# Optimization experiments

Measured on AMD Instinct MI355X. Metric: run time of the kernel, lower is better.

The kernel has to match this reference:

```python
import jax, jax.numpy as jnp
import numpy as np

B, S, D = 8, 4096, 64
LN_EPS = 1e-3  # keras LayerNormalization default epsilon


def setup_inputs() -> dict:
    key = jax.random.key(0)
    k1, k2 = jax.random.split(key)
    x = jax.random.normal(k1, (B, S, D), dtype=jnp.float32)
    # (D,D,D) concept tensor, scaled small like glorot-ish init
    concept_map = jax.random.normal(k2, (D, D, D), dtype=jnp.float32) * 0.02
    gamma = jnp.ones((D,), dtype=jnp.float32)
    beta = jnp.zeros((D,), dtype=jnp.float32)
    return {"x": x, "concept_map": concept_map, "gamma": gamma, "beta": beta}


def reference(x, concept_map, gamma, beta):
    b, s, d = x.shape
    # Causal Toeplitz decay matrix: T[i, j] = 1/(i-j)^2 for j < i, else 0.
    idx = jnp.arange(s)
    diff = idx[:, None] - idx[None, :]  # (S, S)
    T = jnp.where(diff > 0, 1.0 / (jnp.maximum(diff, 1).astype(x.dtype) ** 2), 0.0)
    # Weighted causal prefix sum: S_pre[b, i, c] = sum_{j<i} x[b, j, c] / (i-j)^2
    s_pre = jnp.einsum('ij,bjc->bic', T, x)
    # Bilinear form with concept tensor: out[b,i,k] = sum_{a,c} x[b,i,a] * s_pre[b,i,c] * W[k,a,c]
    outer = (x[:, :, :, None] * s_pre[:, :, None, :]).reshape(b, s, d * d)  # (B,S,D*D)
    out = outer @ concept_map.reshape(d, d * d).T  # (B,S,D)
    # Residual + LayerNorm (axis=-1, keras defaults). Dropout is identity at inference.
    r = out + x
    mu = jnp.mean(r, axis=-1, keepdims=True)
    var = jnp.mean((r - mu) ** 2, axis=-1, keepdims=True)
    y = (r - mu) / jnp.sqrt(var + LN_EPS) * gamma + beta
    return y
```

## Files before the change

### kernel.cpp

```cpp
#include <hip/hip_runtime.h>

#define S_DIM 4096
#define B_DIM 8
#define LN_EPS 1e-3f

typedef _Float16 half8 __attribute__((ext_vector_type(8)));
typedef _Float16 half2v __attribute__((ext_vector_type(2)));
typedef float f32x4 __attribute__((ext_vector_type(4)));

__global__ __launch_bounds__(256) void prep_stage1(const float* __restrict__ x,
                                                   const float* __restrict__ W,
                                                   _Float16* __restrict__ wt2,
                                                   _Float16* __restrict__ s_out) {
    if (blockIdx.x < 1024) {
        int idx = blockIdx.x * 256 + threadIdx.x;
        int a = idx >> 12;
        int j = (idx >> 9) & 7;
        int l2 = (idx >> 3) & 63;
        int e = idx & 7;
        int k = (j >> 1) * 16 + (l2 & 15);
        int c = (j & 1) * 32 + (l2 >> 4) * 8 + e;
        wt2[idx] = (_Float16)W[((k << 6) + a) * 64 + c];
        return;
    }
    const int lin = blockIdx.x - 1024;
    const int it = lin & 63;
    const int by = lin >> 6;
    const int i0 = it * 64;
    const int tid = threadIdx.x;
    const int w = tid >> 6, l = tid & 63, lg = l >> 4, lr = l & 15;

    __shared__ _Float16 Bs[64 * 72];

    f32x4 acc[4] = {};
    const float iRowF = (float)(i0 + w * 16 + lr);
    const int ldC = tid & 63;
    const int ldJ = (tid >> 6) * 16;

    const int jt0 = (it >= 2) ? (it - 2) : 0;
    for (int jt = jt0; jt <= it; ++jt) {
        const int j0 = jt * 64;
        __syncthreads();
        {
            const float* xp = x + ((size_t)by * S_DIM + j0 + ldJ) * 64 + ldC;
            half8 v0, v1;
            #pragma unroll
            for (int q = 0; q < 8; ++q) {
                v0[q] = (_Float16)xp[q * 64];
                v1[q] = (_Float16)xp[(8 + q) * 64];
            }
            *(half8*)&Bs[ldC * 72 + ldJ] = v0;
            *(half8*)&Bs[ldC * 72 + ldJ + 8] = v1;
        }
        __syncthreads();
        #pragma unroll
        for (int kk = 0; kk < 2; ++kk) {
            half8 af;
            #pragma unroll
            for (int bq = 0; bq < 8; ++bq) {
                int j = j0 + kk * 32 + lg * 8 + bq;
                float df = iRowF - (float)j;
                float tv = (df > 0.f) ? __builtin_amdgcn_rcpf(df * df) : 0.f;
                af[bq] = (_Float16)tv;
            }
            #pragma unroll
            for (int nt = 0; nt < 4; ++nt) {
                half8 bf = *(const half8*)&Bs[(nt * 16 + lr) * 72 + kk * 32 + lg * 8];
                acc[nt] = __builtin_amdgcn_mfma_f32_16x16x32_f16(af, bf, acc[nt], 0, 0, 0);
            }
        }
    }

    #pragma unroll
    for (int nt = 0; nt < 4; ++nt)
        #pragma unroll
        for (int r = 0; r < 4; ++r)
            s_out[((size_t)by * S_DIM + i0 + w * 16 + lg * 4 + r) * 64 + nt * 16 + lr]
                = (_Float16)acc[nt][r];
}

__global__ __launch_bounds__(256, 2) void stage2(const float* __restrict__ x,
                                                 const _Float16* __restrict__ s,
                                                 const _Float16* __restrict__ wt2,
                                                 const float* __restrict__ gamma,
                                                 const float* __restrict__ beta,
                                                 float* __restrict__ out) {
    const int r0 = blockIdx.x * 64;
    const int tid = threadIdx.x;
    const int w = tid >> 6, l = tid & 63, lg = l >> 4, lr = l & 15;

    __shared__ __align__(16) half2v Pf[6144];

    const char* mylane = (const char*)wt2 + ((size_t)w << 17) + l * 16;

    half8 sf[4][2];
    #pragma unroll
    for (int rt = 0; rt < 4; ++rt) {
        size_t row = (size_t)(r0 + rt * 16 + lr) * 64;
        sf[rt][0] = *(const half8*)&s[row + lg * 8];
        sf[rt][1] = *(const half8*)&s[row + 32 + lg * 8];
    }
    half8 xav[4][2];
    #pragma unroll
    for (int rt = 0; rt < 4; ++rt) {
        const float* xp = x + (size_t)(r0 + rt * 16 + lr) * 64 + w * 16;
        half8 h0, h1;
        #pragma unroll
        for (int j = 0; j < 8; ++j) {
            h0[j] = (_Float16)xp[j];
            h1[j] = (_Float16)xp[8 + j];
        }
        xav[rt][0] = h0;
        xav[rt][1] = h1;
    }

    half8 bA[4][2], bB[4][2];

#define PREF(BUF, t_)                                                          \
    {                                                                          \
        _Pragma("unroll")                                                      \
        for (int f_ = 0; f_ < 8; ++f_)                                         \
            (&BUF[0][0])[f_] =                                                 \
                *(const half8*)(mylane + (size_t)(t_) * 8192 + f_ * 1024);     \
    }
#define CLUSTER(BUF, t_)                                                       \
    {                                                                          \
        _Pragma("unroll")                                                      \
        for (int rt_ = 0; rt_ < 4; ++rt_) {                                    \
            _Float16 xa = xav[rt_][(t_) >> 3][(t_) & 7];                       \
            half8 af0 = sf[rt_][0] * xa;                                       \
            half8 af1 = sf[rt_][1] * xa;                                       \
            _Pragma("unroll")                                                  \
            for (int nt_ = 0; nt_ < 4; ++nt_) {                                \
                acc[rt_][nt_] = __builtin_amdgcn_mfma_f32_16x16x32_f16(        \
                    af0, BUF[nt_][0], acc[rt_][nt_], 0, 0, 0);                 \
                acc[rt_][nt_] = __builtin_amdgcn_mfma_f32_16x16x32_f16(        \
                    af1, BUF[nt_][1], acc[rt_][nt_], 0, 0, 0);                 \
            }                                                                  \
        }                                                                      \
    }

    f32x4 acc[4][4] = {};
    PREF(bA, 0);
    #pragma unroll
    for (int tt = 0; tt < 8; ++tt) {
        const int t0 = tt * 2;
        PREF(bB, t0 + 1);
        CLUSTER(bA, t0);
        if (t0 + 2 < 16) PREF(bA, t0 + 2);
        CLUSTER(bB, t0 + 1);
    }
#undef PREF
#undef CLUSTER

    if (w != 0) {
        const int ph = w - 1;
        #pragma unroll
        for (int rt = 0; rt < 4; ++rt)
            #pragma unroll
            for (int nt = 0; nt < 4; ++nt) {
                int base = (((ph * 4 + rt) * 4 + nt) * 2) * 64 + l;
                half2v p01 = { (_Float16)acc[rt][nt][0], (_Float16)acc[rt][nt][1] };
                half2v p23 = { (_Float16)acc[rt][nt][2], (_Float16)acc[rt][nt][3] };
                Pf[base] = p01;
                Pf[base + 64] = p23;
            }
    }
    __syncthreads();

    if (w == 0) {
        float gba[4], bta[4];
        #pragma unroll
        for (int nt = 0; nt < 4; ++nt) {
            gba[nt] = gamma[nt * 16 + lr];
            bta[nt] = beta[nt * 16 + lr];
        }
        #pragma unroll
        for (int rt = 0; rt < 4; ++rt) {
            float rv[4][4], sum[4], ssq[4];
            #pragma unroll
            for (int nt = 0; nt < 4; ++nt) {
                float v0 = acc[rt][nt][0], v1 = acc[rt][nt][1];
                float v2 = acc[rt][nt][2], v3 = acc[rt][nt][3];
                #pragma unroll
                for (int ph = 0; ph < 3; ++ph) {
                    int base = (((ph * 4 + rt) * 4 + nt) * 2) * 64 + l;
                    half2v q01 = Pf[base];
                    half2v q23 = Pf[base + 64];
                    v0 += (float)q01[0]; v1 += (float)q01[1];
                    v2 += (float)q23[0]; v3 += (float)q23[1];
                }
                acc[rt][nt][0] = v0; acc[rt][nt][1] = v1;
                acc[rt][nt][2] = v2; acc[rt][nt][3] = v3;
            }
            #pragma unroll
            for (int reg = 0; reg < 4; ++reg) {
                const int row_l = rt * 16 + lg * 4 + reg;
                const float* xr = x + (size_t)(r0 + row_l) * 64;
                float s_ = 0.f, q_ = 0.f;
                #pragma unroll
                for (int nt = 0; nt < 4; ++nt) {
                    float v = acc[rt][nt][reg] + xr[nt * 16 + lr];
                    rv[nt][reg] = v;
                    s_ += v;
                    q_ += v * v;
                }
                sum[reg] = s_;
                ssq[reg] = q_;
            }
            #pragma unroll
            for (int m = 1; m < 16; m <<= 1) {
                #pragma unroll
                for (int reg = 0; reg < 4; ++reg) {
                    sum[reg] += __shfl_xor(sum[reg], m, 64);
                    ssq[reg] += __shfl_xor(ssq[reg], m, 64);
                }
            }
            #pragma unroll
            for (int reg = 0; reg < 4; ++reg) {
                float mean = sum[reg] * (1.f / 64.f);
                float var = ssq[reg] * (1.f / 64.f) - mean * mean;
                float rstd = __frsqrt_rn(var + LN_EPS);
                const int gr = r0 + rt * 16 + lg * 4 + reg;
                #pragma unroll
                for (int nt = 0; nt < 4; ++nt) {
                    float y = (rv[nt][reg] - mean) * rstd * gba[nt] + bta[nt];
                    out[(size_t)gr * 64 + nt * 16 + lr] = y;
                }
            }
        }
    }
}

extern "C" void kernel_launch(void* const* d_in, const int* in_sizes, int n_in,
                              void* d_out, int out_size, void* d_ws, size_t ws_size,
                              hipStream_t stream) {
    const float* x     = (const float*)d_in[0];
    const float* W     = (const float*)d_in[1];
    const float* gamma = (const float*)d_in[2];
    const float* beta  = (const float*)d_in[3];
    float* outp        = (float*)d_out;

    char* ws = (char*)d_ws;
    _Float16* s_f16 = (_Float16*)ws;
    _Float16* wt2   = (_Float16*)(ws + (size_t)B_DIM * S_DIM * 64 * 2);

    prep_stage1<<<1536, 256, 0, stream>>>(x, W, wt2, s_f16);
    stage2<<<(B_DIM * S_DIM) / 64, 256, 0, stream>>>(x, s_f16, wt2, gamma, beta, outp);
}
```

Before: 34.61 us.

## Widen stage2 to 128 rows x 8 waves with LDS staging and tree reduction

The bilinear stage2 kernel now processes 128 rows per block with 8 waves, each handling 8 of the 64 'a' slices instead of 16. The s and x tiles are staged through swizzled LDS rather than held in registers. Each weight fragment loaded from global memory is reused across twice as many rows, which halves weight traffic per row. Per-wave partial sums are combined by a multi-step LDS tree reduction, and the LayerNorm epilogue is spread across all waves with vectorized loads and stores. In exchange the block uses about 68KB of LDS, has more barriers, and doubles the accumulator registers per thread, which may limit occupancy.

```diff
diff --git a/kernel.cpp b/kernel.cpp
--- a/kernel.cpp
+++ b/kernel.cpp
@@ -5,7 +5,7 @@
 #define LN_EPS 1e-3f
 
 typedef _Float16 half8 __attribute__((ext_vector_type(8)));
-typedef _Float16 half2v __attribute__((ext_vector_type(2)));
+typedef _Float16 half4v __attribute__((ext_vector_type(4)));
 typedef float f32x4 __attribute__((ext_vector_type(4)));
 
 __global__ __launch_bounds__(256) void prep_stage1(const float* __restrict__ x,
@@ -79,43 +79,25 @@
                 = (_Float16)acc[nt][r];
 }
 
-__global__ __launch_bounds__(256, 2) void stage2(const float* __restrict__ x,
+__global__ __launch_bounds__(512, 2) void stage2(const float* __restrict__ x,
                                                  const _Float16* __restrict__ s,
                                                  const _Float16* __restrict__ wt2,
                                                  const float* __restrict__ gamma,
                                                  const float* __restrict__ beta,
                                                  float* __restrict__ out) {
-    const int r0 = blockIdx.x * 64;
+    const int r0 = blockIdx.x * 128;
     const int tid = threadIdx.x;
     const int w = tid >> 6, l = tid & 63, lg = l >> 4, lr = l & 15;
 
-    __shared__ __align__(16) half2v Pf[6144];
-
-    const char* mylane = (const char*)wt2 + ((size_t)w << 17) + l * 16;
-
-    half8 sf[4][2];
-    #pragma unroll
-    for (int rt = 0; rt < 4; ++rt) {
-        size_t row = (size_t)(r0 + rt * 16 + lr) * 64;
-        sf[rt][0] = *(const half8*)&s[row + lg * 8];
-        sf[rt][1] = *(const half8*)&s[row + 32 + lg * 8];
-    }
-    half8 xav[4][2];
-    #pragma unroll
-    for (int rt = 0; rt < 4; ++rt) {
-        const float* xp = x + (size_t)(r0 + rt * 16 + lr) * 64 + w * 16;
-        half8 h0, h1;
-        #pragma unroll
-        for (int j = 0; j < 8; ++j) {
-            h0[j] = (_Float16)xp[j];
-            h1[j] = (_Float16)xp[8 + j];
-        }
-        xav[rt][0] = h0;
-        xav[rt][1] = h1;
-    }
+    __shared__ __align__(16) char smem[69632];
+    _Float16* sT = (_Float16*)smem;
+    _Float16* xT = (_Float16*)(smem + 16384);
+
+#define TB(q_) ((_Float16*)(smem + (q_) * 17408))
+
+    const char* mylane = (const char*)wt2 + ((size_t)w << 16) + l * 16;
 
     half8 bA[4][2], bB[4][2];
-
 #define PREF(BUF, t_)                                                          \
     {                                                                          \
         _Pragma("unroll")                                                      \
@@ -123,13 +105,44 @@
             (&BUF[0][0])[f_] =                                                 \
                 *(const half8*)(mylane + (size_t)(t_) * 8192 + f_ * 1024);     \
     }
+
+    PREF(bA, 0);
+
+    {
+        #pragma unroll
+        for (int h = 0; h < 2; ++h) {
+            int slot = h * 512 + tid;
+            int row = slot >> 3, c0 = (slot & 7) * 8;
+            half8 sv = *(const half8*)&s[(size_t)(r0 + row) * 64 + c0];
+            *(half8*)&sT[row * 64 + ((((c0 >> 3) ^ (row & 7))) << 3)] = sv;
+            const float* xp = x + (size_t)(r0 + row) * 64 + c0;
+            float4 v0 = *(const float4*)xp;
+            float4 v1 = *(const float4*)(xp + 4);
+            half8 hv;
+            hv[0] = (_Float16)v0.x; hv[1] = (_Float16)v0.y;
+            hv[2] = (_Float16)v0.z; hv[3] = (_Float16)v0.w;
+            hv[4] = (_Float16)v1.x; hv[5] = (_Float16)v1.y;
+            hv[6] = (_Float16)v1.z; hv[7] = (_Float16)v1.w;
+            *(half8*)&xT[row * 72 + c0] = hv;
+        }
+    }
+    __syncthreads();
+
+    const int sw0 = ((lg ^ (lr & 7)) << 3);
+    const int sw1 = (((4 + lg) ^ (lr & 7)) << 3);
+
+    f32x4 acc[8][4] = {};
+
 #define CLUSTER(BUF, t_)                                                       \
     {                                                                          \
         _Pragma("unroll")                                                      \
-        for (int rt_ = 0; rt_ < 4; ++rt_) {                                    \
-            _Float16 xa = xav[rt_][(t_) >> 3][(t_) & 7];                       \
-            half8 af0 = sf[rt_][0] * xa;                                       \
-            half8 af1 = sf[rt_][1] * xa;                                       \
+        for (int rt_ = 0; rt_ < 8; ++rt_) {                                    \
+            const int row_ = rt_ * 16 + lr;                                    \
+            _Float16 xa = xT[row_ * 72 + w * 8 + (t_)];                        \
+            half8 s0 = *(const half8*)&sT[row_ * 64 + sw0];                    \
+            half8 s1 = *(const half8*)&sT[row_ * 64 + sw1];                    \
+            half8 af0 = s0 * xa;                                               \
+            half8 af1 = s1 * xa;                                               \
             _Pragma("unroll")                                                  \
             for (int nt_ = 0; nt_ < 4; ++nt_) {                                \
                 acc[rt_][nt_] = __builtin_amdgcn_mfma_f32_16x16x32_f16(        \
@@ -140,96 +153,95 @@
         }                                                                      \
     }
 
-    f32x4 acc[4][4] = {};
-    PREF(bA, 0);
     #pragma unroll
-    for (int tt = 0; tt < 8; ++tt) {
+    for (int tt = 0; tt < 4; ++tt) {
         const int t0 = tt * 2;
         PREF(bB, t0 + 1);
         CLUSTER(bA, t0);
-        if (t0 + 2 < 16) PREF(bA, t0 + 2);
+        if (t0 + 2 < 8) PREF(bA, t0 + 2);
         CLUSTER(bB, t0 + 1);
     }
 #undef PREF
 #undef CLUSTER
 
-    if (w != 0) {
-        const int ph = w - 1;
-        #pragma unroll
-        for (int rt = 0; rt < 4; ++rt)
-            #pragma unroll
-            for (int nt = 0; nt < 4; ++nt) {
-                int base = (((ph * 4 + rt) * 4 + nt) * 2) * 64 + l;
-                half2v p01 = { (_Float16)acc[rt][nt][0], (_Float16)acc[rt][nt][1] };
-                half2v p23 = { (_Float16)acc[rt][nt][2], (_Float16)acc[rt][nt][3] };
-                Pf[base] = p01;
-                Pf[base + 64] = p23;
-            }
-    }
-    __syncthreads();
-
-    if (w == 0) {
-        float gba[4], bta[4];
-        #pragma unroll
-        for (int nt = 0; nt < 4; ++nt) {
-            gba[nt] = gamma[nt * 16 + lr];
-            bta[nt] = beta[nt * 16 + lr];
-        }
-        #pragma unroll
-        for (int rt = 0; rt < 4; ++rt) {
-            float rv[4][4], sum[4], ssq[4];
-            #pragma unroll
-            for (int nt = 0; nt < 4; ++nt) {
-                float v0 = acc[rt][nt][0], v1 = acc[rt][nt][1];
-                float v2 = acc[rt][nt][2], v3 = acc[rt][nt][3];
-                #pragma unroll
-                for (int ph = 0; ph < 3; ++ph) {
-                    int base = (((ph * 4 + rt) * 4 + nt) * 2) * 64 + l;
-                    half2v q01 = Pf[base];
-                    half2v q23 = Pf[base + 64];
-                    v0 += (float)q01[0]; v1 += (float)q01[1];
-                    v2 += (float)q23[0]; v3 += (float)q23[1];
-                }
-                acc[rt][nt][0] = v0; acc[rt][nt][1] = v1;
-                acc[rt][nt][2] = v2; acc[rt][nt][3] = v3;
-            }
-            #pragma unroll
-            for (int reg = 0; reg < 4; ++reg) {
-                const int row_l = rt * 16 + lg * 4 + reg;
-                const float* xr = x + (size_t)(r0 + row_l) * 64;
-                float s_ = 0.f, q_ = 0.f;
-                #pragma unroll
-                for (int nt = 0; nt < 4; ++nt) {
-                    float v = acc[rt][nt][reg] + xr[nt * 16 + lr];
-                    rv[nt][reg] = v;
-                    s_ += v;
-                    q_ += v * v;
-                }
-                sum[reg] = s_;
-                ssq[reg] = q_;
-            }
-            #pragma unroll
-            for (int m = 1; m < 16; m <<= 1) {
-                #pragma unroll
-                for (int reg = 0; reg < 4; ++reg) {
-                    sum[reg] += __shfl_xor(sum[reg], m, 64);
-                    ssq[reg] += __shfl_xor(ssq[reg], m, 64);
-                }
-            }
-            #pragma unroll
-            for (int reg = 0; reg < 4; ++reg) {
-                float mean = sum[reg] * (1.f / 64.f);
-                float var = ssq[reg] * (1.f / 64.f) - mean * mean;
-                float rstd = __frsqrt_rn(var + LN_EPS);
-                const int gr = r0 + rt * 16 + lg * 4 + reg;
-                #pragma unroll
-                for (int nt = 0; nt < 4; ++nt) {
-                    float y = (rv[nt][reg] - mean) * rstd * gba[nt] + bta[nt];
-                    out[(size_t)gr * 64 + nt * 16 + lr] = y;
-                }
-            }
-        }
-    }
+#define WRITEP(q_)                                                             \
+    {                                                                          \
+        _Float16* P_ = TB(q_);                                                 \
+        _Pragma("unroll")                                                      \
+        for (int rt_ = 0; rt_ < 8; ++rt_)                                      \
+            _Pragma("unroll")                                                  \
+            for (int nt_ = 0; nt_ < 4; ++nt_)                                  \
+                _Pragma("unroll")                                              \
+                for (int rg_ = 0; rg_ < 4; ++rg_)                              \
+                    P_[(rt_ * 16 + lg * 4 + rg_) * 68 + nt_ * 16 + lr] =       \
+                        (_Float16)acc[rt_][nt_][rg_];                          \
+    }
+#define ADDP(q_)                                                               \
+    {                                                                          \
+        const _Float16* P_ = TB(q_);                                           \
+        _Pragma("unroll")                                                      \
+        for (int rt_ = 0; rt_ < 8; ++rt_)                                      \
+            _Pragma("unroll")                                                  \
+            for (int nt_ = 0; nt_ < 4; ++nt_)                                  \
+                _Pragma("unroll")                                              \
+                for (int rg_ = 0; rg_ < 4; ++rg_)                              \
+                    acc[rt_][nt_][rg_] +=                                      \
+                        (float)P_[(rt_ * 16 + lg * 4 + rg_) * 68 + nt_ * 16 + lr]; \
+    }
+
+    __syncthreads();
+    if (w >= 4) WRITEP(w - 4);
+    __syncthreads();
+    if (w < 4) ADDP(w);
+    __syncthreads();
+    if (w == 2 || w == 3) WRITEP(w - 2);
+    __syncthreads();
+    if (w < 2) ADDP(w);
+    __syncthreads();
+    if (w == 1) WRITEP(0);
+    __syncthreads();
+    if (w == 0) { ADDP(0); WRITEP(1); }
+    __syncthreads();
+#undef WRITEP
+#undef ADDP
+
+    {
+        const int row = w * 16 + (l >> 2);
+        const int q = l & 3;
+        const _Float16* F = TB(1) + row * 68 + q * 16;
+        const float* xr = x + (size_t)(r0 + row) * 64 + q * 16;
+        float v[16];
+        #pragma unroll
+        for (int j = 0; j < 4; ++j) {
+            half4v hv = *(const half4v*)&F[j * 4];
+            float4 xv = *(const float4*)&xr[j * 4];
+            v[j * 4 + 0] = (float)hv[0] + xv.x;
+            v[j * 4 + 1] = (float)hv[1] + xv.y;
+            v[j * 4 + 2] = (float)hv[2] + xv.z;
+            v[j * 4 + 3] = (float)hv[3] + xv.w;
+        }
+        float s_ = 0.f, q2 = 0.f;
+        #pragma unroll
+        for (int i = 0; i < 16; ++i) { s_ += v[i]; q2 += v[i] * v[i]; }
+        s_ += __shfl_xor(s_, 1, 64);  q2 += __shfl_xor(q2, 1, 64);
+        s_ += __shfl_xor(s_, 2, 64);  q2 += __shfl_xor(q2, 2, 64);
+        const float mean = s_ * (1.f / 64.f);
+        const float var = q2 * (1.f / 64.f) - mean * mean;
+        const float rstd = __frsqrt_rn(var + LN_EPS);
+        float* op = out + (size_t)(r0 + row) * 64 + q * 16;
+        #pragma unroll
+        for (int j = 0; j < 4; ++j) {
+            float4 g = *(const float4*)&gamma[q * 16 + j * 4];
+            float4 b = *(const float4*)&beta[q * 16 + j * 4];
+            float4 o;
+            o.x = (v[j * 4 + 0] - mean) * rstd * g.x + b.x;
+            o.y = (v[j * 4 + 1] - mean) * rstd * g.y + b.y;
+            o.z = (v[j * 4 + 2] - mean) * rstd * g.z + b.z;
+            o.w = (v[j * 4 + 3] - mean) * rstd * g.w + b.w;
+            *(float4*)&op[j * 4] = o;
+        }
+    }
+#undef TB
 }
 
 extern "C" void kernel_launch(void* const* d_in, const int* in_sizes, int n_in,
@@ -246,5 +258,5 @@
     _Float16* wt2   = (_Float16*)(ws + (size_t)B_DIM * S_DIM * 64 * 2);
 
     prep_stage1<<<1536, 256, 0, stream>>>(x, W, wt2, s_f16);
-    stage2<<<(B_DIM * S_DIM) / 64, 256, 0, stream>>>(x, s_f16, wt2, gamma, beta, outp);
+    stage2<<<(B_DIM * S_DIM) / 128, 512, 0, stream>>>(x, s_f16, wt2, gamma, beta, outp);
 }
```

Result: slower. 45.50 us (+31.5%).
